# Performance work log

Measured on AMD Instinct MI355X. Metric: run time of the kernel, lower is better.

## Reference

```python
import jax, jax.numpy as jnp
import numpy as np

B, N, F, H, HEADS = 2, 256, 64, 64, 4
C = HEADS * H  # n_coefficients (coefficients_mlp is Identity => must equal n_heads*hidden)
EPS = 1e-5
INF = 1e5


def _lin(key, fan_in, fan_out, bias=True):
    k1, k2 = jax.random.split(key)
    w = jax.random.normal(k1, (fan_in, fan_out), jnp.float32) * (1.0 / np.sqrt(fan_in))
    if bias:
        b = jax.random.normal(k2, (fan_out,), jnp.float32) * 0.01
        return w, b
    return w


def setup_inputs() -> dict:
    key = jax.random.key(0)
    ks = jax.random.split(key, 16)
    inp = dict(
        h=jax.random.normal(ks[0], (B, N, F), jnp.float32),
        x=jax.random.normal(ks[1], (B, N, 3), jnp.float32),
        v=jax.random.normal(ks[2], (B, N, 3), jnp.float32),
    )
    inp['edge_w1'], inp['edge_b1'] = _lin(ks[3], 2 * F + 1, H)
    inp['edge_w2'], inp['edge_b2'] = _lin(ks[4], H, H)
    inp['sem_w'], inp['sem_b'] = _lin(ks[5], H, HEADS)
    inp['post_w1'], inp['post_b1'] = _lin(ks[6], C, H)
    inp['post_w2'], inp['post_b2'] = _lin(ks[7], H, H)
    inp['node_w1'], inp['node_b1'] = _lin(ks[8], C + H + F, H)
    inp['node_w2'], inp['node_b2'] = _lin(ks[9], H, F)
    inp['vel_w1'], inp['vel_b1'] = _lin(ks[10], F, H)
    inp['vel_w2'] = _lin(ks[11], H, 1, bias=False) * 0.001  # xavier gain=0.001 analogue
    inp['vmix_w'] = _lin(ks[12], C, 1, bias=False)[:, 0]
    inp['log_gamma'] = -jnp.log(jnp.linspace(1.0, 5.0, HEADS)).astype(jnp.float32)
    return inp


def reference(h, x, v, edge_w1, edge_b1, edge_w2, edge_b2, sem_w, sem_b,
              post_w1, post_b1, post_w2, post_b2, node_w1, node_b1,
              node_w2, node_b2, vel_w1, vel_b1, vel_w2, vmix_w, log_gamma):
    silu = jax.nn.silu
    n = h.shape[-2]
    eye = jnp.eye(n, dtype=h.dtype)[:, :, None]  # [N,N,1] diagonal mask

    # pairwise geometry: entry [i,j] = x_j - x_i
    x_minus_xt = x[..., None, :, :] - x[..., :, None, :]                # [B,N,N,3]
    x_norm = jnp.sqrt((x_minus_xt ** 2).sum(-1, keepdims=True) + EPS)   # [B,N,N,1]

    # pairwise node-feature concat (h_j, h_i) + distance -> edge MLP
    h_j = jnp.broadcast_to(h[..., None, :, :], (B, n, n, F))
    h_i = jnp.broadcast_to(h[..., :, None, :], (B, n, n, F))
    h_cat = jnp.concatenate([h_j, h_i, x_norm], axis=-1)                # [B,N,N,2F+1]
    h_e_mtx = silu(silu(h_cat @ edge_w1 + edge_b1) @ edge_w2 + edge_b2)  # [B,N,N,H]

    # euclidean attention: softmin over j of gamma*dist, diagonal masked out
    dist = (x_norm + INF * eye) * jnp.exp(log_gamma)                    # [B,N,N,heads]
    euclid_att = jax.nn.softmax(-dist, axis=-2)
    # semantic attention: LeakyReLU(0.2) logits, diagonal masked, softmax over j
    sem = jax.nn.leaky_relu(h_e_mtx @ sem_w + sem_b, 0.2) - INF * eye
    sem_att = jax.nn.softmax(sem, axis=-2)
    comb_att = jax.nn.softmax(euclid_att * sem_att, axis=-2)            # [B,N,N,heads]

    # attention-weighted edge features, flattened over (H, heads)
    h_e_att = (h_e_mtx[..., :, None] * comb_att[..., None, :]).reshape(B, n, n, C)

    # spatial attention (coefficients_mlp is Identity)
    unit = x_minus_xt / (x_norm + EPS)                                  # [B,N,N,3]
    # combinations.mean(dim=-3) without materializing [B,N,N,C,3]
    comb_sum = jnp.einsum('bijc,bijd->bicd', h_e_att, unit) / n         # [B,N,C,3]
    comb_norm = (comb_sum ** 2).sum(-1)                                 # [B,N,C]
    h_comb = silu(silu(comb_norm @ post_w1 + post_b1) @ post_w2 + post_b2)

    # delta_v = mean_j (v_mixing over C of combinations)
    delta_v = jnp.einsum('bijc,c,bijd->bid', h_e_att, vmix_w, unit) / n  # [B,N,3]

    h_agg = h_e_att.sum(axis=-2)                                        # sum over j -> [B,N,C]
    out = jnp.concatenate([h, h_agg, h_comb], axis=-1)
    out = silu(silu(out @ node_w1 + node_b1) @ node_w2 + node_b2)
    h_new = h + out                                                     # residual

    # coordinate / velocity update
    v_scale = silu(h_new @ vel_w1 + vel_b1) @ vel_w2                    # [B,N,1]
    v_new = delta_v + v_scale * v
    x_new = x + v_new
    return h_new, x_new, v_new
```

## Files before the change

kernel.cpp:

```cpp
#include <hip/hip_runtime.h>
#include <hip/hip_bf16.h>
#include <math.h>

#define EPSV 1e-5f
#define INFV 1e5f

typedef short bf16x8 __attribute__((ext_vector_type(8)));
typedef float f32x4 __attribute__((ext_vector_type(4)));

__device__ __forceinline__ float rcp_f(float x) { return __builtin_amdgcn_rcpf(x); }
__device__ __forceinline__ float silu_f(float v) { return v * rcp_f(1.0f + __expf(-v)); }

__device__ __forceinline__ unsigned short f2bf(float f) {
  unsigned int u = __float_as_uint(f);
  u = (u + 0x7fffu + ((u >> 16) & 1u)) >> 16;
  return (unsigned short)u;
}
__device__ __forceinline__ float bf2f(unsigned short h) {
  return __uint_as_float(((unsigned int)h) << 16);
}
__device__ __forceinline__ unsigned int pkbf(float a, float b) {
  float2 f2; f2.x = a; f2.y = b;
  __hip_bfloat162 t = __float22bfloat162_rn(f2);
  unsigned int u;
  __builtin_memcpy(&u, &t, 4);
  return u;
}

__device__ __forceinline__ float4 br4(float4 v, int op, float4* sc) {
  const int tid = threadIdx.x;
#pragma unroll
  for (int off = 32; off >= 1; off >>= 1) {
    float ox = __shfl_xor(v.x, off);
    float oy = __shfl_xor(v.y, off);
    float oz = __shfl_xor(v.z, off);
    float ow = __shfl_xor(v.w, off);
    if (op) { v.x = fmaxf(v.x, ox); v.y = fmaxf(v.y, oy); v.z = fmaxf(v.z, oz); v.w = fmaxf(v.w, ow); }
    else    { v.x += ox; v.y += oy; v.z += oz; v.w += ow; }
  }
  if ((tid & 63) == 0) sc[tid >> 6] = v;
  __syncthreads();
  float4 r0 = sc[0], r1 = sc[1], r2 = sc[2], r3 = sc[3];
  if (op) {
    v.x = fmaxf(fmaxf(r0.x, r1.x), fmaxf(r2.x, r3.x));
    v.y = fmaxf(fmaxf(r0.y, r1.y), fmaxf(r2.y, r3.y));
    v.z = fmaxf(fmaxf(r0.z, r1.z), fmaxf(r2.z, r3.z));
    v.w = fmaxf(fmaxf(r0.w, r1.w), fmaxf(r2.w, r3.w));
  } else {
    v.x = r0.x + r1.x + r2.x + r3.x;
    v.y = r0.y + r1.y + r2.y + r3.y;
    v.z = r0.z + r1.z + r2.z + r3.z;
    v.w = r0.w + r1.w + r2.w + r3.w;
  }
  __syncthreads();
  return v;
}

__device__ __forceinline__ void gemm64(const unsigned short* TH, const unsigned short* E2T,
                                       int w, int l15, int quad, f32x4 acc[4][4]) {
#pragma unroll
  for (int tr = 0; tr < 4; ++tr)
#pragma unroll
    for (int tc = 0; tc < 4; ++tc)
      acc[tr][tc] = (f32x4){0.f, 0.f, 0.f, 0.f};
#pragma unroll
  for (int ms = 0; ms < 64; ms += 32) {
    bf16x8 af[4], bfr[4];
#pragma unroll
    for (int tr = 0; tr < 4; ++tr)
      af[tr] = *reinterpret_cast<const bf16x8*>(&TH[(64 * w + 16 * tr + l15) * 72 + ms + quad * 8]);
#pragma unroll
    for (int tc = 0; tc < 4; ++tc)
      bfr[tc] = *reinterpret_cast<const bf16x8*>(&E2T[(16 * tc + l15) * 72 + ms + quad * 8]);
#pragma unroll
    for (int tr = 0; tr < 4; ++tr)
#pragma unroll
      for (int tc = 0; tc < 4; ++tc)
        acc[tr][tc] = __builtin_amdgcn_mfma_f32_16x16x32_bf16(af[tr], bfr[tc], acc[tr][tc], 0, 0, 0);
  }
}

__global__ __launch_bounds__(256, 3) void k_all(
    const float* __restrict__ h, const float* __restrict__ x, const float* __restrict__ v,
    const float* __restrict__ ew1, const float* __restrict__ eb1,
    const float* __restrict__ ew2, const float* __restrict__ eb2,
    const float* __restrict__ semw, const float* __restrict__ semb,
    const float* __restrict__ pw1, const float* __restrict__ pb1,
    const float* __restrict__ pw2, const float* __restrict__ pb2,
    const float* __restrict__ nw1, const float* __restrict__ nb1,
    const float* __restrict__ nw2, const float* __restrict__ nb2,
    const float* __restrict__ vw1, const float* __restrict__ vb1,
    const float* __restrict__ vw2, const float* __restrict__ vmix,
    const float* __restrict__ lgam, float* __restrict__ out) {

  __shared__ __align__(16) unsigned short TH[256 * 72];
  __shared__ __align__(16) char E2u[9216];
  __shared__ __align__(16) float4 unit_l[256];
  __shared__ float addk[64];
  __shared__ float w1dk[64];
  __shared__ __align__(16) float bms[256];

  unsigned short* E2T = (unsigned short*)E2u;
  float*  sd    = (float*)E2u;
  float4* cat_l = (float4*)E2u;
  float*  cn_l  = (float*)(E2u + 4096);
  float*  hag_l = (float*)(E2u + 5120);
  float4* sc    = (float4*)(E2u + 8192);
  float*  dvs   = (float*)(E2u + 8320);
  float* tmp = (float*)TH;
  float* m1s = (float*)TH + 256;
  float* hnw = (float*)TH + 320;
  float* nin = (float*)TH + 384;

  const int bi  = blockIdx.x;
  const int i   = bi & 255;
  const int b0  = bi & ~255;
  const int tid = threadIdx.x;
  const int j   = tid;
  const int bj  = b0 | j;

  const float xi0 = x[bi * 3 + 0], xi1 = x[bi * 3 + 1], xi2 = x[bi * 3 + 2];
  const float dx = x[bj * 3 + 0] - xi0;
  const float dy = x[bj * 3 + 1] - xi1;
  const float dz = x[bj * 3 + 2] - xi2;
  const float dn = sqrtf(dx * dx + dy * dy + dz * dz + EPSV);
  const float invn = rcp_f(dn + EPSV);
  const float ux = dx * invn, uy = dy * invn, uz = dz * invn;
  unit_l[j] = make_float4(ux, uy, uz, dn);

  {
    const float4* hb4 = reinterpret_cast<const float4*>(h + (size_t)b0 * 64);
#pragma unroll
    for (int q = 0; q < 16; ++q) {
      int idx = q * 256 + tid;
      float4 f4 = hb4[idx];
      int row = idx >> 4, c4 = idx & 15;
      uint2 pk;
      pk.x = pkbf(f4.x, f4.y);
      pk.y = pkbf(f4.z, f4.w);
      *reinterpret_cast<uint2*>(&TH[row * 72 + c4 * 4]) = pk;
    }
  }
#pragma unroll
  for (int q = 0; q < 16; ++q) {
    int idx = q * 256 + tid;
    E2T[(idx & 63) * 72 + (idx >> 6)] = f2bf(ew1[idx]);
  }
  {
    int s = tid >> 6, k = tid & 63;
    const float* hrow = h + (size_t)bi * 64;
    float bp = 0.f;
#pragma unroll
    for (int f2 = 0; f2 < 16; ++f2) {
      int f = s * 16 + f2;
      bp += hrow[f] * ew1[(64 + f) * 64 + k];
    }
    bms[s * 64 + k] = bp;
  }
  __syncthreads();
  if (tid < 64) {
    addk[tid] = eb1[tid] + bms[tid] + bms[64 + tid] + bms[128 + tid] + bms[192 + tid];
    w1dk[tid] = ew1[128 * 64 + tid];
  }

  const int lid  = tid & 63;
  const int w    = tid >> 6;
  const int l15  = lid & 15;
  const int quad = lid >> 4;

  f32x4 acc[4][4];
  gemm64(TH, E2T, w, l15, quad, acc);
  __syncthreads();

#pragma unroll
  for (int tc = 0; tc < 4; ++tc) {
    float ak = addk[16 * tc + l15];
    float wd = w1dk[16 * tc + l15];
#pragma unroll
    for (int tr = 0; tr < 4; ++tr)
#pragma unroll
      for (int r = 0; r < 4; ++r) {
        int row = 64 * w + 16 * tr + quad * 4 + r;
        float val = silu_f(acc[tr][tc][r] + ak + unit_l[row].w * wd);
        TH[row * 72 + 16 * tc + l15] = f2bf(val);
      }
  }
#pragma unroll
  for (int q = 0; q < 16; ++q) {
    int idx = q * 256 + tid;
    E2T[(idx & 63) * 72 + (idx >> 6)] = f2bf(ew2[idx]);
  }
  __syncthreads();

  gemm64(TH, E2T, w, l15, quad, acc);
  __syncthreads();

#pragma unroll
  for (int tc = 0; tc < 4; ++tc) {
    float b2 = eb2[16 * tc + l15];
#pragma unroll
    for (int tr = 0; tr < 4; ++tr)
#pragma unroll
      for (int r = 0; r < 4; ++r) {
        int row = 64 * w + 16 * tr + quad * 4 + r;
        TH[row * 72 + 16 * tc + l15] = f2bf(silu_f(acc[tr][tc][r] + b2));
      }
  }
#pragma unroll
  for (int q = 0; q < 2; ++q) {
    int idx = q * 256 + tid;
    int n = idx >> 6, kk = idx & 63;
    float wv = (n < 4) ? semw[kk * 4 + n] : vmix[kk * 4 + (n - 4)];
    E2T[n * 72 + kk] = f2bf(wv);
  }
  __syncthreads();

  f32x4 acc3[4];
  {
#pragma unroll
    for (int tr = 0; tr < 4; ++tr) acc3[tr] = (f32x4){0.f, 0.f, 0.f, 0.f};
#pragma unroll
    for (int ms = 0; ms < 64; ms += 32) {
      bf16x8 b3 = *reinterpret_cast<const bf16x8*>(&E2T[l15 * 72 + ms + quad * 8]);
#pragma unroll
      for (int tr = 0; tr < 4; ++tr) {
        bf16x8 a3 = *reinterpret_cast<const bf16x8*>(&TH[(64 * w + 16 * tr + l15) * 72 + ms + quad * 8]);
        acc3[tr] = __builtin_amdgcn_mfma_f32_16x16x32_bf16(a3, b3, acc3[tr], 0, 0, 0);
      }
    }
  }
  __syncthreads();
  if (l15 < 8) {
#pragma unroll
    for (int tr = 0; tr < 4; ++tr)
#pragma unroll
      for (int r = 0; r < 4; ++r)
        sd[(64 * w + 16 * tr + quad * 4 + r) * 8 + l15] = acc3[tr][r];
  }
  __syncthreads();

  float4 s01 = *reinterpret_cast<const float4*>(sd + j * 8);
  float4 s23 = *reinterpret_cast<const float4*>(sd + j * 8 + 4);
  float4 sbv = *reinterpret_cast<const float4*>(semb);
  const float diag = (j == i) ? INFV : 0.0f;
  float4 sl;
  sl.x = s01.x + sbv.x; sl.y = s01.y + sbv.y; sl.z = s01.z + sbv.z; sl.w = s01.w + sbv.w;
  sl.x = ((sl.x > 0.f) ? sl.x : 0.2f * sl.x) - diag;
  sl.y = ((sl.y > 0.f) ? sl.y : 0.2f * sl.y) - diag;
  sl.z = ((sl.z > 0.f) ? sl.z : 0.2f * sl.z) - diag;
  sl.w = ((sl.w > 0.f) ? sl.w : 0.2f * sl.w) - diag;

  float4 lg = *reinterpret_cast<const float4*>(lgam);
  const float dni = dn + diag;
  float4 e_eu = make_float4(__expf(-dni * __expf(lg.x)), __expf(-dni * __expf(lg.y)),
                            __expf(-dni * __expf(lg.z)), __expf(-dni * __expf(lg.w)));

  float4 M = br4(sl, 1, sc);
  float4 e_sem = make_float4(__expf(sl.x - M.x), __expf(sl.y - M.y),
                             __expf(sl.z - M.z), __expf(sl.w - M.w));

  float4 a8 = e_eu, b8 = e_sem;
#pragma unroll
  for (int off = 32; off >= 1; off >>= 1) {
    a8.x += __shfl_xor(a8.x, off); a8.y += __shfl_xor(a8.y, off);
    a8.z += __shfl_xor(a8.z, off); a8.w += __shfl_xor(a8.w, off);
    b8.x += __shfl_xor(b8.x, off); b8.y += __shfl_xor(b8.y, off);
    b8.z += __shfl_xor(b8.z, off); b8.w += __shfl_xor(b8.w, off);
  }
  if ((tid & 63) == 0) { sc[tid >> 6] = a8; sc[4 + (tid >> 6)] = b8; }
  __syncthreads();
  float4 Se, Ss;
  {
    float4 r0 = sc[0], r1 = sc[1], r2 = sc[2], r3 = sc[3];
    Se = make_float4(r0.x + r1.x + r2.x + r3.x, r0.y + r1.y + r2.y + r3.y,
                     r0.z + r1.z + r2.z + r3.z, r0.w + r1.w + r2.w + r3.w);
    float4 s0 = sc[4], s1 = sc[5], s2 = sc[6], s3 = sc[7];
    Ss = make_float4(s0.x + s1.x + s2.x + s3.x, s0.y + s1.y + s2.y + s3.y,
                     s0.z + s1.z + s2.z + s3.z, s0.w + s1.w + s2.w + s3.w);
  }
  __syncthreads();

  float4 p = make_float4((e_eu.x * rcp_f(Se.x)) * (e_sem.x * rcp_f(Ss.x)),
                         (e_eu.y * rcp_f(Se.y)) * (e_sem.y * rcp_f(Ss.y)),
                         (e_eu.z * rcp_f(Se.z)) * (e_sem.z * rcp_f(Ss.z)),
                         (e_eu.w * rcp_f(Se.w)) * (e_sem.w * rcp_f(Ss.w)));
  float4 ep = make_float4(__expf(p.x), __expf(p.y), __expf(p.z), __expf(p.w));
  float4 Sp = br4(ep, 0, sc);
  float4 catt = make_float4(ep.x * rcp_f(Sp.x), ep.y * rcp_f(Sp.y),
                            ep.z * rcp_f(Sp.z), ep.w * rcp_f(Sp.w));
  cat_l[j] = catt;

  float s = catt.x * s23.x + catt.y * s23.y + catt.z * s23.z + catt.w * s23.w;
  float4 dv = br4(make_float4(s * ux, s * uy, s * uz, 0.f), 0, sc);
  if (j == 0) {
    const float inv = 1.0f / 256.0f;
    dvs[0] = dv.x * inv; dvs[1] = dv.y * inv; dvs[2] = dv.z * inv;
  }

  {
    const int kk = lid & 15;
    const int jq = lid >> 4;
    const int k  = 16 * w + kk;
    float agg[4] = {0.f, 0.f, 0.f, 0.f};
    float ax[4]  = {0.f, 0.f, 0.f, 0.f};
    float ay[4]  = {0.f, 0.f, 0.f, 0.f};
    float az[4]  = {0.f, 0.f, 0.f, 0.f};
#pragma unroll 4
    for (int jr2 = 0; jr2 < 64; ++jr2) {
      int jj = jq * 64 + ((jr2 + 4 * jq) & 63);
      float hev = bf2f(TH[jj * 72 + k]);
      float4 ca = cat_l[jj];
      float4 u  = unit_l[jj];
      float w0 = hev * ca.x, w1 = hev * ca.y, w2 = hev * ca.z, w3 = hev * ca.w;
      agg[0] += w0; agg[1] += w1; agg[2] += w2; agg[3] += w3;
      ax[0] += w0 * u.x; ay[0] += w0 * u.y; az[0] += w0 * u.z;
      ax[1] += w1 * u.x; ay[1] += w1 * u.y; az[1] += w1 * u.z;
      ax[2] += w2 * u.x; ay[2] += w2 * u.y; az[2] += w2 * u.z;
      ax[3] += w3 * u.x; ay[3] += w3 * u.y; az[3] += w3 * u.z;
    }
#pragma unroll
    for (int off = 16; off <= 32; off <<= 1) {
#pragma unroll
      for (int hd = 0; hd < 4; ++hd) {
        agg[hd] += __shfl_xor(agg[hd], off);
        ax[hd]  += __shfl_xor(ax[hd], off);
        ay[hd]  += __shfl_xor(ay[hd], off);
        az[hd]  += __shfl_xor(az[hd], off);
      }
    }
    if (jq == 0) {
      const float inv = 1.0f / 256.0f;
#pragma unroll
      for (int hd = 0; hd < 4; ++hd) {
        float cx = ax[hd] * inv, cy = ay[hd] * inv, cz = az[hd] * inv;
        cn_l[k * 4 + hd]  = cx * cx + cy * cy + cz * cz;
        hag_l[k * 4 + hd] = agg[hd];
      }
    }
  }
  __syncthreads();

  const int k = tid & 63;
  {
    float a = 0.f;
    for (int m2 = 0; m2 < 64; ++m2) {
      int m = w * 64 + m2;
      a += cn_l[m] * pw1[m * 64 + k];
    }
    tmp[tid] = a;
  }
  __syncthreads();
  if (tid < 64) m1s[tid] = silu_f(pb1[tid] + tmp[tid] + tmp[64 + tid] + tmp[128 + tid] + tmp[192 + tid]);
  __syncthreads();
  {
    float a = 0.f;
#pragma unroll
    for (int m2 = 0; m2 < 16; ++m2) {
      int m = w * 16 + m2;
      a += m1s[m] * pw2[m * 64 + k];
    }
    float hgv = hag_l[tid];
    __syncthreads();
    tmp[tid] = a;
    nin[64 + tid] = hgv;
  }
  __syncthreads();
  if (tid < 64) {
    nin[tid] = h[(size_t)bi * 64 + tid];
    nin[320 + tid] = silu_f(pb2[tid] + tmp[tid] + tmp[64 + tid] + tmp[128 + tid] + tmp[192 + tid]);
  }
  __syncthreads();
  {
    float a = 0.f;
    for (int m2 = 0; m2 < 96; ++m2) {
      int m = w * 96 + m2;
      a += nin[m] * nw1[m * 64 + k];
    }
    __syncthreads();
    tmp[tid] = a;
  }
  __syncthreads();
  if (tid < 64) m1s[tid] = silu_f(nb1[tid] + tmp[tid] + tmp[64 + tid] + tmp[128 + tid] + tmp[192 + tid]);
  __syncthreads();
  {
    float a = 0.f;
#pragma unroll
    for (int m2 = 0; m2 < 16; ++m2) {
      int m = w * 16 + m2;
      a += m1s[m] * nw2[m * 64 + k];
    }
    __syncthreads();
    tmp[tid] = a;
  }
  __syncthreads();
  if (tid < 64) {
    float hn = h[(size_t)bi * 64 + tid] +
               silu_f(nb2[tid] + tmp[tid] + tmp[64 + tid] + tmp[128 + tid] + tmp[192 + tid]);
    out[(size_t)bi * 64 + tid] = hn;
    hnw[tid] = hn;
  }
  __syncthreads();
  {
    float a = 0.f;
#pragma unroll
    for (int m2 = 0; m2 < 16; ++m2) {
      int m = w * 16 + m2;
      a += hnw[m] * vw1[m * 64 + k];
    }
    __syncthreads();
    tmp[tid] = a;
  }
  __syncthreads();
  if (tid < 64) {
    float vh = silu_f(vb1[tid] + tmp[tid] + tmp[64 + tid] + tmp[128 + tid] + tmp[192 + tid]) * vw2[tid];
#pragma unroll
    for (int off = 32; off >= 1; off >>= 1) vh += __shfl_xor(vh, off);
    if (tid == 0) {
#pragma unroll
      for (int d = 0; d < 3; ++d) {
        float vn = dvs[d] + vh * v[bi * 3 + d];
        out[32768 + bi * 3 + d] = x[bi * 3 + d] + vn;
        out[34304 + bi * 3 + d] = vn;
      }
    }
  }
}

extern "C" void kernel_launch(void* const* d_in, const int* in_sizes, int n_in,
                              void* d_out, int out_size, void* d_ws, size_t ws_size,
                              hipStream_t stream) {
  const float* h    = (const float*)d_in[0];
  const float* x    = (const float*)d_in[1];
  const float* v    = (const float*)d_in[2];
  const float* ew1  = (const float*)d_in[3];
  const float* eb1  = (const float*)d_in[4];
  const float* ew2  = (const float*)d_in[5];
  const float* eb2  = (const float*)d_in[6];
  const float* semw = (const float*)d_in[7];
  const float* semb = (const float*)d_in[8];
  const float* pw1  = (const float*)d_in[9];
  const float* pb1  = (const float*)d_in[10];
  const float* pw2  = (const float*)d_in[11];
  const float* pb2  = (const float*)d_in[12];
  const float* nw1  = (const float*)d_in[13];
  const float* nb1  = (const float*)d_in[14];
  const float* nw2  = (const float*)d_in[15];
  const float* nb2  = (const float*)d_in[16];
  const float* vw1  = (const float*)d_in[17];
  const float* vb1  = (const float*)d_in[18];
  const float* vw2  = (const float*)d_in[19];
  const float* vmix = (const float*)d_in[20];
  const float* lgam = (const float*)d_in[21];
  float* out = (float*)d_out;

  k_all<<<512, 256, 0, stream>>>(h, x, v, ew1, eb1, ew2, eb2, semw, semb,
                                 pw1, pb1, pw2, pb2, nw1, nb1, nw2, nb2,
                                 vw1, vb1, vw2, vmix, lgam, out);
}
```

Before: 121.9 us.

## Move per-channel j-aggregation to MFMA with transposed edge features and fused reductions

```diff
diff --git a/kernel.cpp b/kernel.cpp
--- a/kernel.cpp
+++ b/kernel.cpp
@@ -27,35 +27,6 @@
   return u;
 }
 
-__device__ __forceinline__ float4 br4(float4 v, int op, float4* sc) {
-  const int tid = threadIdx.x;
-#pragma unroll
-  for (int off = 32; off >= 1; off >>= 1) {
-    float ox = __shfl_xor(v.x, off);
-    float oy = __shfl_xor(v.y, off);
-    float oz = __shfl_xor(v.z, off);
-    float ow = __shfl_xor(v.w, off);
-    if (op) { v.x = fmaxf(v.x, ox); v.y = fmaxf(v.y, oy); v.z = fmaxf(v.z, oz); v.w = fmaxf(v.w, ow); }
-    else    { v.x += ox; v.y += oy; v.z += oz; v.w += ow; }
-  }
-  if ((tid & 63) == 0) sc[tid >> 6] = v;
-  __syncthreads();
-  float4 r0 = sc[0], r1 = sc[1], r2 = sc[2], r3 = sc[3];
-  if (op) {
-    v.x = fmaxf(fmaxf(r0.x, r1.x), fmaxf(r2.x, r3.x));
-    v.y = fmaxf(fmaxf(r0.y, r1.y), fmaxf(r2.y, r3.y));
-    v.z = fmaxf(fmaxf(r0.z, r1.z), fmaxf(r2.z, r3.z));
-    v.w = fmaxf(fmaxf(r0.w, r1.w), fmaxf(r2.w, r3.w));
-  } else {
-    v.x = r0.x + r1.x + r2.x + r3.x;
-    v.y = r0.y + r1.y + r2.y + r3.y;
-    v.z = r0.z + r1.z + r2.z + r3.z;
-    v.w = r0.w + r1.w + r2.w + r3.w;
-  }
-  __syncthreads();
-  return v;
-}
-
 __device__ __forceinline__ void gemm64(const unsigned short* TH, const unsigned short* E2T,
                                        int w, int l15, int quad, f32x4 acc[4][4]) {
 #pragma unroll
@@ -80,7 +51,7 @@
   }
 }
 
-__global__ __launch_bounds__(256, 3) void k_all(
+__global__ __launch_bounds__(256, 2) void k_all(
     const float* __restrict__ h, const float* __restrict__ x, const float* __restrict__ v,
     const float* __restrict__ ew1, const float* __restrict__ eb1,
     const float* __restrict__ ew2, const float* __restrict__ eb2,
@@ -93,24 +64,25 @@
     const float* __restrict__ vw2, const float* __restrict__ vmix,
     const float* __restrict__ lgam, float* __restrict__ out) {
 
-  __shared__ __align__(16) unsigned short TH[256 * 72];
-  __shared__ __align__(16) char E2u[9216];
-  __shared__ __align__(16) float4 unit_l[256];
-  __shared__ float addk[64];
-  __shared__ float w1dk[64];
+  __shared__ __align__(16) unsigned short THu[256 * 72];
+  __shared__ __align__(16) unsigned short E2u[64 * 72];
+  __shared__ __align__(16) float dn_l[256];
+  __shared__ __align__(16) float comps[64 * 12];
+  __shared__ __align__(16) float cn_l[256];
+  __shared__ __align__(16) float hag_l[256];
   __shared__ __align__(16) float bms[256];
-
-  unsigned short* E2T = (unsigned short*)E2u;
-  float*  sd    = (float*)E2u;
-  float4* cat_l = (float4*)E2u;
-  float*  cn_l  = (float*)(E2u + 4096);
-  float*  hag_l = (float*)(E2u + 5120);
-  float4* sc    = (float4*)(E2u + 8192);
-  float*  dvs   = (float*)(E2u + 8320);
-  float* tmp = (float*)TH;
-  float* m1s = (float*)TH + 256;
-  float* hnw = (float*)TH + 320;
-  float* nin = (float*)TH + 384;
+  __shared__ __align__(16) float addk[64];
+  __shared__ __align__(16) float w1dk[64];
+  __shared__ __align__(16) float4 sc[8];
+
+  unsigned short* TH  = THu;
+  unsigned short* HEt = THu;
+  unsigned short* E2T = E2u;
+  unsigned short* Bt  = E2u;
+  float* tmp = (float*)THu;
+  float* m1s = (float*)THu + 256;
+  float* hnw = (float*)THu + 320;
+  float* nin = (float*)THu + 384;
 
   const int bi  = blockIdx.x;
   const int i   = bi & 255;
@@ -118,6 +90,10 @@
   const int tid = threadIdx.x;
   const int j   = tid;
   const int bj  = b0 | j;
+  const int w    = tid >> 6;
+  const int lid  = tid & 63;
+  const int l15  = lid & 15;
+  const int quad = lid >> 4;
 
   const float xi0 = x[bi * 3 + 0], xi1 = x[bi * 3 + 1], xi2 = x[bi * 3 + 2];
   const float dx = x[bj * 3 + 0] - xi0;
@@ -126,7 +102,7 @@
   const float dn = sqrtf(dx * dx + dy * dy + dz * dz + EPSV);
   const float invn = rcp_f(dn + EPSV);
   const float ux = dx * invn, uy = dy * invn, uz = dz * invn;
-  unit_l[j] = make_float4(ux, uy, uz, dn);
+  dn_l[j] = dn;
 
   {
     const float4* hb4 = reinterpret_cast<const float4*>(h + (size_t)b0 * 64);
@@ -163,11 +139,6 @@
     w1dk[tid] = ew1[128 * 64 + tid];
   }
 
-  const int lid  = tid & 63;
-  const int w    = tid >> 6;
-  const int l15  = lid & 15;
-  const int quad = lid >> 4;
-
   f32x4 acc[4][4];
   gemm64(TH, E2T, w, l15, quad, acc);
   __syncthreads();
@@ -181,7 +152,7 @@
 #pragma unroll
       for (int r = 0; r < 4; ++r) {
         int row = 64 * w + 16 * tr + quad * 4 + r;
-        float val = silu_f(acc[tr][tc][r] + ak + unit_l[row].w * wd);
+        float val = silu_f(acc[tr][tc][r] + ak + dn_l[row] * wd);
         TH[row * 72 + 16 * tc + l15] = f2bf(val);
       }
   }
@@ -192,59 +163,54 @@
   }
   __syncthreads();
 
-  gemm64(TH, E2T, w, l15, quad, acc);
-  __syncthreads();
-
+  {
+    bf16x8 a2[4][2], b2[4][2];
+#pragma unroll
+    for (int tr = 0; tr < 4; ++tr)
+#pragma unroll
+      for (int ms = 0; ms < 2; ++ms)
+        a2[tr][ms] = *reinterpret_cast<const bf16x8*>(&TH[(64 * w + 16 * tr + l15) * 72 + ms * 32 + quad * 8]);
+#pragma unroll
+    for (int tc = 0; tc < 4; ++tc)
+#pragma unroll
+      for (int ms = 0; ms < 2; ++ms)
+        b2[tc][ms] = *reinterpret_cast<const bf16x8*>(&E2T[(16 * tc + l15) * 72 + ms * 32 + quad * 8]);
+    __syncthreads();
+#pragma unroll
+    for (int tr = 0; tr < 4; ++tr)
+#pragma unroll
+      for (int tc = 0; tc < 4; ++tc)
+        acc[tr][tc] = (f32x4){0.f, 0.f, 0.f, 0.f};
+#pragma unroll
+    for (int ms = 0; ms < 2; ++ms)
+#pragma unroll
+      for (int tr = 0; tr < 4; ++tr)
+#pragma unroll
+        for (int tc = 0; tc < 4; ++tc)
+          acc[tr][tc] = __builtin_amdgcn_mfma_f32_16x16x32_bf16(a2[tr][ms], b2[tc][ms], acc[tr][tc], 0, 0, 0);
+  }
 #pragma unroll
   for (int tc = 0; tc < 4; ++tc) {
-    float b2 = eb2[16 * tc + l15];
+    float b2v = eb2[16 * tc + l15];
+    int ch = 16 * tc + l15;
 #pragma unroll
     for (int tr = 0; tr < 4; ++tr)
 #pragma unroll
       for (int r = 0; r < 4; ++r) {
         int row = 64 * w + 16 * tr + quad * 4 + r;
-        TH[row * 72 + 16 * tc + l15] = f2bf(silu_f(acc[tr][tc][r] + b2));
+        HEt[ch * 264 + row] = f2bf(silu_f(acc[tr][tc][r] + b2v));
       }
   }
-#pragma unroll
-  for (int q = 0; q < 2; ++q) {
-    int idx = q * 256 + tid;
-    int n = idx >> 6, kk = idx & 63;
-    float wv = (n < 4) ? semw[kk * 4 + n] : vmix[kk * 4 + (n - 4)];
-    E2T[n * 72 + kk] = f2bf(wv);
-  }
-  __syncthreads();
-
-  f32x4 acc3[4];
-  {
-#pragma unroll
-    for (int tr = 0; tr < 4; ++tr) acc3[tr] = (f32x4){0.f, 0.f, 0.f, 0.f};
-#pragma unroll
-    for (int ms = 0; ms < 64; ms += 32) {
-      bf16x8 b3 = *reinterpret_cast<const bf16x8*>(&E2T[l15 * 72 + ms + quad * 8]);
-#pragma unroll
-      for (int tr = 0; tr < 4; ++tr) {
-        bf16x8 a3 = *reinterpret_cast<const bf16x8*>(&TH[(64 * w + 16 * tr + l15) * 72 + ms + quad * 8]);
-        acc3[tr] = __builtin_amdgcn_mfma_f32_16x16x32_bf16(a3, b3, acc3[tr], 0, 0, 0);
-      }
-    }
-  }
-  __syncthreads();
-  if (l15 < 8) {
-#pragma unroll
-    for (int tr = 0; tr < 4; ++tr)
-#pragma unroll
-      for (int r = 0; r < 4; ++r)
-        sd[(64 * w + 16 * tr + quad * 4 + r) * 8 + l15] = acc3[tr][r];
-  }
-  __syncthreads();
-
-  float4 s01 = *reinterpret_cast<const float4*>(sd + j * 8);
-  float4 s23 = *reinterpret_cast<const float4*>(sd + j * 8 + 4);
-  float4 sbv = *reinterpret_cast<const float4*>(semb);
+  __syncthreads();
+
+  float4 sl = *reinterpret_cast<const float4*>(semb);
+#pragma unroll 8
+  for (int ch = 0; ch < 64; ++ch) {
+    float he = bf2f(HEt[ch * 264 + tid]);
+    const float4 swv = *reinterpret_cast<const float4*>(semw + ch * 4);
+    sl.x += he * swv.x; sl.y += he * swv.y; sl.z += he * swv.z; sl.w += he * swv.w;
+  }
   const float diag = (j == i) ? INFV : 0.0f;
-  float4 sl;
-  sl.x = s01.x + sbv.x; sl.y = s01.y + sbv.y; sl.z = s01.z + sbv.z; sl.w = s01.w + sbv.w;
   sl.x = ((sl.x > 0.f) ? sl.x : 0.2f * sl.x) - diag;
   sl.y = ((sl.y > 0.f) ? sl.y : 0.2f * sl.y) - diag;
   sl.z = ((sl.z > 0.f) ? sl.z : 0.2f * sl.z) - diag;
@@ -255,90 +221,120 @@
   float4 e_eu = make_float4(__expf(-dni * __expf(lg.x)), __expf(-dni * __expf(lg.y)),
                             __expf(-dni * __expf(lg.z)), __expf(-dni * __expf(lg.w)));
 
-  float4 M = br4(sl, 1, sc);
+  float4 M, Se;
+  {
+    float4 m4 = sl, s4 = e_eu;
+#pragma unroll
+    for (int off = 32; off >= 1; off >>= 1) {
+      m4.x = fmaxf(m4.x, __shfl_xor(m4.x, off)); m4.y = fmaxf(m4.y, __shfl_xor(m4.y, off));
+      m4.z = fmaxf(m4.z, __shfl_xor(m4.z, off)); m4.w = fmaxf(m4.w, __shfl_xor(m4.w, off));
+      s4.x += __shfl_xor(s4.x, off); s4.y += __shfl_xor(s4.y, off);
+      s4.z += __shfl_xor(s4.z, off); s4.w += __shfl_xor(s4.w, off);
+    }
+    if (lid == 0) { sc[w] = m4; sc[4 + w] = s4; }
+    __syncthreads();
+    float4 r0 = sc[0], r1 = sc[1], r2 = sc[2], r3 = sc[3];
+    M = make_float4(fmaxf(fmaxf(r0.x, r1.x), fmaxf(r2.x, r3.x)),
+                    fmaxf(fmaxf(r0.y, r1.y), fmaxf(r2.y, r3.y)),
+                    fmaxf(fmaxf(r0.z, r1.z), fmaxf(r2.z, r3.z)),
+                    fmaxf(fmaxf(r0.w, r1.w), fmaxf(r2.w, r3.w)));
+    float4 s0 = sc[4], s1 = sc[5], s2 = sc[6], s3 = sc[7];
+    Se = make_float4(s0.x + s1.x + s2.x + s3.x, s0.y + s1.y + s2.y + s3.y,
+                     s0.z + s1.z + s2.z + s3.z, s0.w + s1.w + s2.w + s3.w);
+    __syncthreads();
+  }
   float4 e_sem = make_float4(__expf(sl.x - M.x), __expf(sl.y - M.y),
                              __expf(sl.z - M.z), __expf(sl.w - M.w));
-
-  float4 a8 = e_eu, b8 = e_sem;
-#pragma unroll
-  for (int off = 32; off >= 1; off >>= 1) {
-    a8.x += __shfl_xor(a8.x, off); a8.y += __shfl_xor(a8.y, off);
-    a8.z += __shfl_xor(a8.z, off); a8.w += __shfl_xor(a8.w, off);
-    b8.x += __shfl_xor(b8.x, off); b8.y += __shfl_xor(b8.y, off);
-    b8.z += __shfl_xor(b8.z, off); b8.w += __shfl_xor(b8.w, off);
-  }
-  if ((tid & 63) == 0) { sc[tid >> 6] = a8; sc[4 + (tid >> 6)] = b8; }
-  __syncthreads();
-  float4 Se, Ss;
-  {
-    float4 r0 = sc[0], r1 = sc[1], r2 = sc[2], r3 = sc[3];
-    Se = make_float4(r0.x + r1.x + r2.x + r3.x, r0.y + r1.y + r2.y + r3.y,
-                     r0.z + r1.z + r2.z + r3.z, r0.w + r1.w + r2.w + r3.w);
-    float4 s0 = sc[4], s1 = sc[5], s2 = sc[6], s3 = sc[7];
+  float4 Ss;
+  {
+    float4 s4 = e_sem;
+#pragma unroll
+    for (int off = 32; off >= 1; off >>= 1) {
+      s4.x += __shfl_xor(s4.x, off); s4.y += __shfl_xor(s4.y, off);
+      s4.z += __shfl_xor(s4.z, off); s4.w += __shfl_xor(s4.w, off);
+    }
+    if (lid == 0) sc[w] = s4;
+    __syncthreads();
+    float4 s0 = sc[0], s1 = sc[1], s2 = sc[2], s3 = sc[3];
     Ss = make_float4(s0.x + s1.x + s2.x + s3.x, s0.y + s1.y + s2.y + s3.y,
                      s0.z + s1.z + s2.z + s3.z, s0.w + s1.w + s2.w + s3.w);
-  }
-  __syncthreads();
-
+    __syncthreads();
+  }
   float4 p = make_float4((e_eu.x * rcp_f(Se.x)) * (e_sem.x * rcp_f(Ss.x)),
                          (e_eu.y * rcp_f(Se.y)) * (e_sem.y * rcp_f(Ss.y)),
                          (e_eu.z * rcp_f(Se.z)) * (e_sem.z * rcp_f(Ss.z)),
                          (e_eu.w * rcp_f(Se.w)) * (e_sem.w * rcp_f(Ss.w)));
   float4 ep = make_float4(__expf(p.x), __expf(p.y), __expf(p.z), __expf(p.w));
-  float4 Sp = br4(ep, 0, sc);
-  float4 catt = make_float4(ep.x * rcp_f(Sp.x), ep.y * rcp_f(Sp.y),
-                            ep.z * rcp_f(Sp.z), ep.w * rcp_f(Sp.w));
-  cat_l[j] = catt;
-
-  float s = catt.x * s23.x + catt.y * s23.y + catt.z * s23.z + catt.w * s23.w;
-  float4 dv = br4(make_float4(s * ux, s * uy, s * uz, 0.f), 0, sc);
-  if (j == 0) {
+  float4 catt;
+  {
+    float4 s4 = ep;
+#pragma unroll
+    for (int off = 32; off >= 1; off >>= 1) {
+      s4.x += __shfl_xor(s4.x, off); s4.y += __shfl_xor(s4.y, off);
+      s4.z += __shfl_xor(s4.z, off); s4.w += __shfl_xor(s4.w, off);
+    }
+    if (lid == 0) sc[w] = s4;
+    __syncthreads();
+    float4 s0 = sc[0], s1 = sc[1], s2 = sc[2], s3 = sc[3];
+    float4 Sp = make_float4(s0.x + s1.x + s2.x + s3.x, s0.y + s1.y + s2.y + s3.y,
+                            s0.z + s1.z + s2.z + s3.z, s0.w + s1.w + s2.w + s3.w);
+    catt = make_float4(ep.x * rcp_f(Sp.x), ep.y * rcp_f(Sp.y),
+                       ep.z * rcp_f(Sp.z), ep.w * rcp_f(Sp.w));
+    __syncthreads();
+  }
+
+  {
+    float cv[4] = {catt.x, catt.y, catt.z, catt.w};
+    float uv[3] = {ux, uy, uz};
+#pragma unroll
+    for (int hd = 0; hd < 4; ++hd) {
+      Bt[hd * 264 + j] = f2bf(cv[hd]);
+#pragma unroll
+      for (int d = 0; d < 3; ++d)
+        Bt[(4 + hd * 3 + d) * 264 + j] = f2bf(cv[hd] * uv[d]);
+    }
+  }
+  __syncthreads();
+
+  {
+    f32x4 a4 = (f32x4){0.f, 0.f, 0.f, 0.f};
+#pragma unroll
+    for (int ks = 0; ks < 8; ++ks) {
+      bf16x8 av = *reinterpret_cast<const bf16x8*>(&HEt[(16 * w + l15) * 264 + ks * 32 + quad * 8]);
+      bf16x8 bv = *reinterpret_cast<const bf16x8*>(&Bt[l15 * 264 + ks * 32 + quad * 8]);
+      a4 = __builtin_amdgcn_mfma_f32_16x16x32_bf16(av, bv, a4, 0, 0, 0);
+    }
     const float inv = 1.0f / 256.0f;
-    dvs[0] = dv.x * inv; dvs[1] = dv.y * inv; dvs[2] = dv.z * inv;
-  }
-
-  {
-    const int kk = lid & 15;
-    const int jq = lid >> 4;
-    const int k  = 16 * w + kk;
-    float agg[4] = {0.f, 0.f, 0.f, 0.f};
-    float ax[4]  = {0.f, 0.f, 0.f, 0.f};
-    float ay[4]  = {0.f, 0.f, 0.f, 0.f};
-    float az[4]  = {0.f, 0.f, 0.f, 0.f};
-#pragma unroll 4
-    for (int jr2 = 0; jr2 < 64; ++jr2) {
-      int jj = jq * 64 + ((jr2 + 4 * jq) & 63);
-      float hev = bf2f(TH[jj * 72 + k]);
-      float4 ca = cat_l[jj];
-      float4 u  = unit_l[jj];
-      float w0 = hev * ca.x, w1 = hev * ca.y, w2 = hev * ca.z, w3 = hev * ca.w;
-      agg[0] += w0; agg[1] += w1; agg[2] += w2; agg[3] += w3;
-      ax[0] += w0 * u.x; ay[0] += w0 * u.y; az[0] += w0 * u.z;
-      ax[1] += w1 * u.x; ay[1] += w1 * u.y; az[1] += w1 * u.z;
-      ax[2] += w2 * u.x; ay[2] += w2 * u.y; az[2] += w2 * u.z;
-      ax[3] += w3 * u.x; ay[3] += w3 * u.y; az[3] += w3 * u.z;
-    }
-#pragma unroll
-    for (int off = 16; off <= 32; off <<= 1) {
-#pragma unroll
-      for (int hd = 0; hd < 4; ++hd) {
-        agg[hd] += __shfl_xor(agg[hd], off);
-        ax[hd]  += __shfl_xor(ax[hd], off);
-        ay[hd]  += __shfl_xor(ay[hd], off);
-        az[hd]  += __shfl_xor(az[hd], off);
-      }
-    }
-    if (jq == 0) {
-      const float inv = 1.0f / 256.0f;
-#pragma unroll
-      for (int hd = 0; hd < 4; ++hd) {
-        float cx = ax[hd] * inv, cy = ay[hd] * inv, cz = az[hd] * inv;
-        cn_l[k * 4 + hd]  = cx * cx + cy * cy + cz * cz;
-        hag_l[k * 4 + hd] = agg[hd];
-      }
-    }
-  }
-  __syncthreads();
+#pragma unroll
+    for (int r = 0; r < 4; ++r) {
+      int ch = 16 * w + quad * 4 + r;
+      if (l15 < 4) hag_l[ch * 4 + l15] = a4[r];
+      else         comps[ch * 12 + (l15 - 4)] = a4[r] * inv;
+    }
+  }
+  __syncthreads();
+
+  float dvx, dvy, dvz;
+  {
+    int chh = tid >> 2, hh = tid & 3;
+    float cx = comps[chh * 12 + hh * 3 + 0];
+    float cy = comps[chh * 12 + hh * 3 + 1];
+    float cz = comps[chh * 12 + hh * 3 + 2];
+    cn_l[tid] = cx * cx + cy * cy + cz * cz;
+    float vmw = vmix[tid];
+    float px = vmw * cx, py = vmw * cy, pz = vmw * cz;
+#pragma unroll
+    for (int off = 32; off >= 1; off >>= 1) {
+      px += __shfl_xor(px, off); py += __shfl_xor(py, off); pz += __shfl_xor(pz, off);
+    }
+    if (lid == 0) sc[w] = make_float4(px, py, pz, 0.f);
+    __syncthreads();
+    float4 r0 = sc[0], r1 = sc[1], r2 = sc[2], r3 = sc[3];
+    dvx = r0.x + r1.x + r2.x + r3.x;
+    dvy = r0.y + r1.y + r2.y + r3.y;
+    dvz = r0.z + r1.z + r2.z + r3.z;
+    __syncthreads();
+  }
 
   const int k = tid & 63;
   {
@@ -416,9 +412,10 @@
 #pragma unroll
     for (int off = 32; off >= 1; off >>= 1) vh += __shfl_xor(vh, off);
     if (tid == 0) {
+      float dvv[3] = {dvx, dvy, dvz};
 #pragma unroll
       for (int d = 0; d < 3; ++d) {
-        float vn = dvs[d] + vh * v[bi * 3 + d];
+        float vn = dvv[d] + vh * v[bi * 3 + d];
         out[32768 + bi * 3 + d] = x[bi * 3 + d] + vn;
         out[34304 + bi * 3 + d] = vn;
       }
```

New measurement: 122.6 us. No clear change (+0.6%).
